# Kernel optimization log

Measured on AMD Instinct MI355X. Metric: run time of the kernel, lower is better.

## Reference

```python
import jax, jax.numpy as jnp
import numpy as np

N_NODES = 3070
N_FEAT = 128
N_OUT = 64
H_SIZE = 50
N_EDGES = 49120
BATCH = 128


def setup_inputs() -> dict:
    key = jax.random.key(0)
    ks = jax.random.split(key, 8)
    x_in = jax.random.normal(ks[0], (BATCH, N_NODES, N_FEAT), dtype=jnp.float32)
    edge_index = jax.random.randint(ks[1], (2, N_EDGES), 0, N_NODES, dtype=jnp.int64)
    edge_weight = jax.random.uniform(ks[2], (N_EDGES,), dtype=jnp.float32)
    W = jax.random.normal(ks[3], (N_FEAT, N_OUT), dtype=jnp.float32) / np.sqrt(N_FEAT)
    b = jnp.zeros((N_OUT,), dtype=jnp.float32)
    W_ih = jax.random.normal(ks[4], (H_SIZE, N_OUT), dtype=jnp.float32) / np.sqrt(N_OUT)
    W_hh = jax.random.normal(ks[5], (H_SIZE, H_SIZE), dtype=jnp.float32) / np.sqrt(H_SIZE)
    b_ih = jnp.zeros((H_SIZE,), dtype=jnp.float32)
    b_hh = jnp.zeros((H_SIZE,), dtype=jnp.float32)
    h0 = jax.random.normal(ks[6], (N_NODES, H_SIZE), dtype=jnp.float32)
    return {"x_in": x_in, "edge_index": edge_index, "edge_weight": edge_weight,
            "W": W, "b": b, "W_ih": W_ih, "W_hh": W_hh, "b_ih": b_ih,
            "b_hh": b_hh, "h0": h0}


def _gcn(x, edge_index, edge_weight, W, b):
    # x: (B, N, F). Vectorized GCNConv over the per-sample python loop.
    n = x.shape[1]
    # vectorized form of the dict-based edge-id remap: rank among unique ids
    uniq = jnp.unique(edge_index, size=n, fill_value=2 ** 30)
    ei = jnp.searchsorted(uniq, edge_index)
    src, dst = ei[0], ei[1]
    # GCNConv default: add self loops with weight 1, symmetric normalization
    loop = jnp.arange(n)
    src = jnp.concatenate([src, loop])
    dst = jnp.concatenate([dst, loop])
    ew = jnp.concatenate([edge_weight, jnp.ones((n,), dtype=x.dtype)])
    deg = jax.ops.segment_sum(ew, dst, num_segments=n)
    dinv = jnp.where(deg > 0, jax.lax.rsqrt(deg), jnp.zeros_like(deg))
    norm = dinv[src] * ew * dinv[dst]                 # (E+N,)
    xw = jnp.einsum('bnf,fo->bno', x, W)              # transform first
    msg = xw[:, src, :] * norm[None, :, None]         # (B, E+N, O)
    out = jnp.zeros_like(xw).at[:, dst, :].add(msg)   # scatter-add to targets
    return out + b


def reference(x_in, edge_index, edge_weight, W, b, W_ih, W_hh, b_ih, b_hh, h0):
    # GCN over all B graph samples (shared fixed graph)
    x = _gcn(x_in, edge_index, edge_weight, W, b)     # (B, N, O)
    # input_horizon==3 -> exactly one horizon step; the torch RNN is seq-first,
    # so seq_len = B (sample dim) and batch = N_NODES, hidden hardcoded 50.
    def step(h, xt):                                   # xt: (N, O), h: (N, H)
        h = jnp.tanh(xt @ W_ih.T + b_ih + h @ W_hh.T + b_hh)
        return h, h
    _, x_out = jax.lax.scan(step, h0, x)               # (B, N, H)
    return x_out
```

## Files before the change

kernel.cpp:

```cpp
#include <hip/hip_runtime.h>

#define NN 3070
#define NF 128
#define NO 64
#define NH 50
#define NC 52
#define NE 49120
#define NB 128
#define MTOT (NB * NN)
#define GCAP 1024
#define NBLK 192
#define GWG2 (NBLK * (NB / 2))
#define GPX2 (GWG2 / 8)

__global__ __launch_bounds__(256) void init_kernel(int* __restrict__ zb,
    const float* __restrict__ W, const float* __restrict__ Wih, const float* __restrict__ b,
    const float* __restrict__ bih, const float* __restrict__ bhh,
    float* __restrict__ Wp, float* __restrict__ bp) {
  int blk = blockIdx.x;
  int tid = threadIdx.x;
  if (blk < 48) {
    int i = blk * 256 + tid;
    if (i < 4 * NN) zb[i] = 0;
    return;
  }
  int idx = (blk - 48) * 256 + tid;
  if (idx < 128 * 64) {
    int k = idx >> 6, j = idx & 63;
    float s = 0.f;
    if (j < NH) {
      for (int o = 0; o < NO; ++o) s += W[k * NO + o] * Wih[j * NO + o];
    }
    Wp[k * 64 + j] = s;
  }
  if (idx < NC) {
    float s = 0.f;
    if (idx < NH) {
      for (int o = 0; o < NO; ++o) s += b[o] * Wih[idx * NO + o];
      s += bih[idx] + bhh[idx];
    }
    bp[idx] = s;
  }
}

__global__ __launch_bounds__(256) void mark_kernel(const int* __restrict__ ei, int* __restrict__ mark) {
  int i = blockIdx.x * 256 + threadIdx.x;
  if (i < 2 * NE) mark[ei[i]] = 1;
}

__global__ __launch_bounds__(1024) void exscan_kernel(const int* __restrict__ in, int* __restrict__ out,
                                                      int n, int write_total, int do_dinv,
                                                      const float* __restrict__ degw,
                                                      float* __restrict__ dinv, float* __restrict__ selfn) {
  __shared__ int part[1024];
  int tid = threadIdx.x;
  int base = tid * 3;
  if (do_dinv) {
#pragma unroll
    for (int u = 0; u < 3; ++u) {
      int nd = base + u;
      if (nd < NN) {
        float dg = degw[nd] + 1.0f;
        float di = rsqrtf(dg);
        dinv[nd] = di;
        selfn[nd] = di * di;
      }
    }
  }
  int v0 = (base + 0 < n) ? in[base + 0] : 0;
  int v1 = (base + 1 < n) ? in[base + 1] : 0;
  int v2 = (base + 2 < n) ? in[base + 2] : 0;
  int s = v0 + v1 + v2;
  part[tid] = s;
  __syncthreads();
  for (int off = 1; off < 1024; off <<= 1) {
    int t = (tid >= off) ? part[tid - off] : 0;
    __syncthreads();
    part[tid] += t;
    __syncthreads();
  }
  int run = part[tid] - s;
  if (base + 0 < n) out[base + 0] = run; run += v0;
  if (base + 1 < n) out[base + 1] = run; run += v1;
  if (base + 2 < n) out[base + 2] = run;
  if (write_total && tid == 1023) out[n] = part[1023];
}

__global__ __launch_bounds__(256) void remap_deg_kernel(const int* __restrict__ ei, const float* __restrict__ ew,
    const int* __restrict__ ranks, int* __restrict__ srcr, int* __restrict__ dstr,
    int* __restrict__ degc, float* __restrict__ degw) {
  int e = blockIdx.x * 256 + threadIdx.x;
  if (e >= NE) return;
  int s = ranks[ei[e]];
  int d = ranks[ei[NE + e]];
  srcr[e] = s;
  dstr[e] = d;
  atomicAdd(&degc[d], 1);
  atomicAdd(&degw[d], ew[e]);
}

__global__ __launch_bounds__(256) void csr_fill_kernel(const float* __restrict__ ew, const int* __restrict__ srcr,
    const int* __restrict__ dstr, const int* __restrict__ rowptr, int* __restrict__ cursor,
    const float* __restrict__ dinv, int* __restrict__ csr_src, float* __restrict__ csr_norm) {
  int e = blockIdx.x * 256 + threadIdx.x;
  if (e >= NE) return;
  int d = dstr[e];
  int s = srcr[e];
  int pos = rowptr[d] + atomicAdd(&cursor[d], 1);
  csr_src[pos] = s;
  csr_norm[pos] = dinv[s] * ew[e] * dinv[d];
}

__global__ __launch_bounds__(256, 3) void gemm_kernel(const float* __restrict__ A,
    const float* __restrict__ W, float* __restrict__ out) {
  __shared__ float As[256 * 36];
  __shared__ float Ws[32 * 64];
  int tid = threadIdx.x;
  int row0 = blockIdx.x * 256;
  int rg = tid >> 3;
  int cg = tid & 7;
  int c0 = cg * 8;
  float acc[8][8];
#pragma unroll
  for (int i = 0; i < 8; ++i)
#pragma unroll
    for (int j = 0; j < 8; ++j) acc[i][j] = 0.f;

  for (int kc = 0; kc < 4; ++kc) {
#pragma unroll
    for (int j = 0; j < 8; ++j) {
      int f = tid + 256 * j;
      int r = f >> 3, kq = f & 7;
      float4 v = *(const float4*)&A[(size_t)(row0 + r) * NF + kc * 32 + kq * 4];
      *(float4*)&As[r * 36 + kq * 4] = v;
    }
#pragma unroll
    for (int j = 0; j < 2; ++j) {
      int f = tid + 256 * j;
      int kk = f >> 4, cq = f & 15;
      *(float4*)&Ws[kk * 64 + cq * 4] = *(const float4*)&W[(size_t)(kc * 32 + kk) * 64 + cq * 4];
    }
    __syncthreads();
#pragma unroll 2
    for (int k4 = 0; k4 < 32; k4 += 4) {
      float4 a[8];
#pragma unroll
      for (int i = 0; i < 8; ++i) a[i] = *(const float4*)&As[(rg + 32 * i) * 36 + k4];
#pragma unroll
      for (int m = 0; m < 4; ++m) {
        float4 w0 = *(const float4*)&Ws[(k4 + m) * 64 + c0];
        float4 w1 = *(const float4*)&Ws[(k4 + m) * 64 + c0 + 4];
#pragma unroll
        for (int i = 0; i < 8; ++i) {
          float av = (m == 0) ? a[i].x : (m == 1) ? a[i].y : (m == 2) ? a[i].z : a[i].w;
          acc[i][0] += av * w0.x; acc[i][1] += av * w0.y;
          acc[i][2] += av * w0.z; acc[i][3] += av * w0.w;
          acc[i][4] += av * w1.x; acc[i][5] += av * w1.y;
          acc[i][6] += av * w1.z; acc[i][7] += av * w1.w;
        }
      }
    }
    __syncthreads();
  }
#pragma unroll
  for (int i = 0; i < 8; ++i) {
    size_t r = row0 + rg + 32 * i;
    if (c0 < NC)
      *(float4*)&out[r * NC + c0] = make_float4(acc[i][0], acc[i][1], acc[i][2], acc[i][3]);
    if (c0 + 4 < NC)
      *(float4*)&out[r * NC + c0 + 4] = make_float4(acc[i][4], acc[i][5], acc[i][6], acc[i][7]);
  }
}

__global__ __launch_bounds__(256) void gather_kernel(const float4* __restrict__ xw,
    const int* __restrict__ rowptr, const int* __restrict__ csr_src, const float* __restrict__ csr_norm,
    const float* __restrict__ selfn, const float* __restrict__ bp, float4* __restrict__ outg) {
  __shared__ int s_src[GCAP];
  __shared__ float s_nrm[GCAP];
  int bid = blockIdx.x;
  int xcd = bid & 7;
  int pos = bid >> 3;
  int work = xcd * GPX2 + pos;
  int bpr = work / NBLK;
  int nblk = work - bpr * NBLK;
  int b0 = bpr * 2;
  int tid = threadIdx.x;
  int f4 = tid & 15, nl = tid >> 4;
  int nb = nblk * 16;
  int nend = nb + 16 < NN ? nb + 16 : NN;
  int be0 = rowptr[nb], be1 = rowptr[nend];
  int cnt = be1 - be0;
  int scnt = cnt < GCAP ? cnt : GCAP;
  for (int i = tid; i < scnt; i += 256) {
    s_src[i] = csr_src[be0 + i];
    s_nrm[i] = csr_norm[be0 + i];
  }
  __syncthreads();
  int n = nb + nl;
  if (n >= NN || f4 >= 13) return;
  const float4* xb0 = xw + (size_t)b0 * NN * 13;
  const float4* xb1 = xb0 + (size_t)NN * 13;
  float sn = selfn[n];
  float4 v0 = xb0[n * 13 + f4];
  float4 v1 = xb1[n * 13 + f4];
  float ax = v0.x * sn, ay = v0.y * sn, az = v0.z * sn, aw = v0.w * sn;
  float bx = 0.f, by = 0.f, bz = 0.f, bw = 0.f;
  float cx = v1.x * sn, cy = v1.y * sn, cz = v1.z * sn, cw = v1.w * sn;
  float dx = 0.f, dy = 0.f, dz = 0.f, dw = 0.f;
  int le0 = rowptr[n] - be0, le1 = rowptr[n + 1] - be0;
  int lim = le1 < GCAP ? le1 : GCAP;
  int e = le0;
  for (; e + 1 < lim; e += 2) {
    int s1 = s_src[e], s2 = s_src[e + 1];
    float w1 = s_nrm[e], w2 = s_nrm[e + 1];
    float4 u10 = xb0[s1 * 13 + f4];
    float4 u20 = xb0[s2 * 13 + f4];
    float4 u11 = xb1[s1 * 13 + f4];
    float4 u21 = xb1[s2 * 13 + f4];
    ax += w1 * u10.x; ay += w1 * u10.y; az += w1 * u10.z; aw += w1 * u10.w;
    bx += w2 * u20.x; by += w2 * u20.y; bz += w2 * u20.z; bw += w2 * u20.w;
    cx += w1 * u11.x; cy += w1 * u11.y; cz += w1 * u11.z; cw += w1 * u11.w;
    dx += w2 * u21.x; dy += w2 * u21.y; dz += w2 * u21.z; dw += w2 * u21.w;
  }
  if (e < lim) {
    int s1 = s_src[e];
    float w1 = s_nrm[e];
    float4 u10 = xb0[s1 * 13 + f4];
    float4 u11 = xb1[s1 * 13 + f4];
    ax += w1 * u10.x; ay += w1 * u10.y; az += w1 * u10.z; aw += w1 * u10.w;
    cx += w1 * u11.x; cy += w1 * u11.y; cz += w1 * u11.z; cw += w1 * u11.w;
  }
  for (e = (le0 > GCAP ? le0 : GCAP); e < le1; ++e) {
    int s1 = csr_src[be0 + e];
    float w1 = csr_norm[be0 + e];
    float4 u10 = xb0[s1 * 13 + f4];
    float4 u11 = xb1[s1 * 13 + f4];
    ax += w1 * u10.x; ay += w1 * u10.y; az += w1 * u10.z; aw += w1 * u10.w;
    cx += w1 * u11.x; cy += w1 * u11.y; cz += w1 * u11.z; cw += w1 * u11.w;
  }
  float4 bb = ((const float4*)bp)[f4];
  float4 o0 = make_float4(ax + bx + bb.x, ay + by + bb.y, az + bz + bb.z, aw + bw + bb.w);
  float4 o1 = make_float4(cx + dx + bb.x, cy + dy + bb.y, cz + dz + bb.z, cw + dw + bb.w);
  outg[((size_t)b0 * NN + n) * 13 + f4] = o0;
  outg[((size_t)(b0 + 1) * NN + n) * 13 + f4] = o1;
}

__global__ __launch_bounds__(256, 3) void rnn_kernel(const float* __restrict__ pre,
    const float* __restrict__ Whh, const float* __restrict__ h0, float* __restrict__ out) {
  __shared__ float hs[6 * 52];
  int tid = threadIdx.x;
  int n0 = blockIdx.x * 5;
  int nl = tid / 50;
  int j = tid - nl * 50;
  bool active = tid < 250;
  int jj = active ? j : 0;
  float2 whh2[25];
  const float2* whhp = (const float2*)(Whh + jj * NH);
#pragma unroll
  for (int q = 0; q < 25; ++q) whh2[q] = whhp[q];
  if (tid < 6 * 52) hs[tid] = 0.f;
  if (tid + 256 < 6 * 52) hs[tid + 256] = 0.f;
  __syncthreads();
  if (active) hs[nl * 52 + j] = h0[n0 * 50 + tid];
  const size_t NPRE = (size_t)NN * NC;
  const size_t NOUT = (size_t)NN * NH;
  int nn = active ? (n0 + nl) : n0;
  const float* prep = pre + (size_t)nn * NC + jj;
  float xpre = prep[0];
  __syncthreads();
  for (int t = 0; t < NB; ++t) {
    float a0 = xpre, a1 = 0.f, a2 = 0.f, a3 = 0.f;
    if (t + 1 < NB) xpre = prep[(size_t)(t + 1) * NPRE];
    const float4* hr = (const float4*)&hs[nl * 52];
#pragma unroll
    for (int q = 0; q < 12; q += 4) {
      float4 h0v = hr[q], h1v = hr[q + 1], h2v = hr[q + 2], h3v = hr[q + 3];
      a0 += h0v.x * whh2[2*q].x   + h0v.y * whh2[2*q].y   + h0v.z * whh2[2*q+1].x + h0v.w * whh2[2*q+1].y;
      a1 += h1v.x * whh2[2*q+2].x + h1v.y * whh2[2*q+2].y + h1v.z * whh2[2*q+3].x + h1v.w * whh2[2*q+3].y;
      a2 += h2v.x * whh2[2*q+4].x + h2v.y * whh2[2*q+4].y + h2v.z * whh2[2*q+5].x + h2v.w * whh2[2*q+5].y;
      a3 += h3v.x * whh2[2*q+6].x + h3v.y * whh2[2*q+6].y + h3v.z * whh2[2*q+7].x + h3v.w * whh2[2*q+7].y;
    }
    {
      float2 ht = *(const float2*)&hs[nl * 52 + 48];
      a0 += ht.x * whh2[24].x + ht.y * whh2[24].y;
    }
    float v = (a0 + a1) + (a2 + a3);
    float e = __expf(-2.f * fabsf(v));
    float r = (1.f - e) * __builtin_amdgcn_rcpf(1.f + e);
    float hnew = (v < 0.f) ? -r : r;
    __syncthreads();
    if (active) {
      hs[nl * 52 + j] = hnew;
      out[(size_t)t * NOUT + n0 * 50 + tid] = hnew;
    }
    __syncthreads();
  }
}


extern "C" void kernel_launch(void* const* d_in, const int* in_sizes, int n_in,
                              void* d_out, int out_size, void* d_ws, size_t ws_size,
                              hipStream_t stream) {
  const float* x_in = (const float*)d_in[0];
  const int* ei     = (const int*)d_in[1];
  const float* ew   = (const float*)d_in[2];
  const float* W    = (const float*)d_in[3];
  const float* bias = (const float*)d_in[4];
  const float* Wih  = (const float*)d_in[5];
  const float* Whh  = (const float*)d_in[6];
  const float* bih  = (const float*)d_in[7];
  const float* bhh  = (const float*)d_in[8];
  const float* h0   = (const float*)d_in[9];
  float* out = (float*)d_out;

  char* ws = (char*)d_ws;
  size_t off = 0;
  auto alloc = [&](size_t bytes) {
    size_t o = off;
    off += (bytes + 255) & ~(size_t)255;
    return o;
  };
  float* xw    = (float*)(ws + alloc((size_t)MTOT * NC * 4));
  float* gcn   = (float*)(ws + alloc((size_t)MTOT * NC * 4));
  int*   zb    = (int*)(ws + alloc((size_t)4 * NN * 4));
  int* mark = zb;
  int* degc = zb + NN;
  float* degw = (float*)(zb + 2 * NN);
  int* cursor = zb + 3 * NN;
  int*   ranks  = (int*)(ws + alloc(NN * 4));
  int*   srcr   = (int*)(ws + alloc(NE * 4));
  int*   dstr   = (int*)(ws + alloc(NE * 4));
  float* dinv   = (float*)(ws + alloc(NN * 4));
  float* selfn  = (float*)(ws + alloc(NN * 4));
  int*   rowptr = (int*)(ws + alloc((NN + 1) * 4));
  int*   csrc   = (int*)(ws + alloc(NE * 4));
  float* cnorm  = (float*)(ws + alloc(NE * 4));
  float* Wp     = (float*)(ws + alloc(128 * 64 * 4));
  float* bp     = (float*)(ws + alloc(NC * 4));

  init_kernel<<<80, 256, 0, stream>>>(zb, W, Wih, bias, bih, bhh, Wp, bp);
  mark_kernel<<<(2 * NE + 255) / 256, 256, 0, stream>>>(ei, mark);
  exscan_kernel<<<1, 1024, 0, stream>>>(mark, ranks, NN, 0, 0, degw, dinv, selfn);
  remap_deg_kernel<<<(NE + 255) / 256, 256, 0, stream>>>(ei, ew, ranks, srcr, dstr, degc, degw);
  exscan_kernel<<<1, 1024, 0, stream>>>(degc, rowptr, NN, 1, 1, degw, dinv, selfn);
  csr_fill_kernel<<<(NE + 255) / 256, 256, 0, stream>>>(ew, srcr, dstr, rowptr, cursor, dinv, csrc, cnorm);

  gemm_kernel<<<MTOT / 256, 256, 0, stream>>>(x_in, Wp, xw);
  gather_kernel<<<GWG2, 256, 0, stream>>>(
      (const float4*)xw, rowptr, csrc, cnorm, selfn, bp, (float4*)gcn);
  rnn_kernel<<<(NN + 4) / 5, 256, 0, stream>>>(gcn, Whh, h0, out);
}
```

Baseline: 536.2 us.

## Stage per-batch feature slice in LDS and gather neighbors from shared memory

```diff
diff --git a/kernel.cpp b/kernel.cpp
--- a/kernel.cpp
+++ b/kernel.cpp
@@ -8,10 +8,8 @@
 #define NE 49120
 #define NB 128
 #define MTOT (NB * NN)
-#define GCAP 1024
-#define NBLK 192
-#define GWG2 (NBLK * (NB / 2))
-#define GPX2 (GWG2 / 8)
+#define GWG3 (7 * NB)
+#define GPX3 (GWG3 / 8)
 
 __global__ __launch_bounds__(256) void init_kernel(int* __restrict__ zb,
     const float* __restrict__ W, const float* __restrict__ Wih, const float* __restrict__ b,
@@ -101,14 +99,14 @@
 
 __global__ __launch_bounds__(256) void csr_fill_kernel(const float* __restrict__ ew, const int* __restrict__ srcr,
     const int* __restrict__ dstr, const int* __restrict__ rowptr, int* __restrict__ cursor,
-    const float* __restrict__ dinv, int* __restrict__ csr_src, float* __restrict__ csr_norm) {
+    const float* __restrict__ dinv, int2* __restrict__ csre) {
   int e = blockIdx.x * 256 + threadIdx.x;
   if (e >= NE) return;
   int d = dstr[e];
   int s = srcr[e];
   int pos = rowptr[d] + atomicAdd(&cursor[d], 1);
-  csr_src[pos] = s;
-  csr_norm[pos] = dinv[s] * ew[e] * dinv[d];
+  float nrm = dinv[s] * ew[e] * dinv[d];
+  csre[pos] = make_int2(2 * s, __float_as_int(nrm));
 }
 
 __global__ __launch_bounds__(256, 3) void gemm_kernel(const float* __restrict__ A,
@@ -172,77 +170,73 @@
   }
 }
 
-__global__ __launch_bounds__(256) void gather_kernel(const float4* __restrict__ xw,
-    const int* __restrict__ rowptr, const int* __restrict__ csr_src, const float* __restrict__ csr_norm,
+__global__ __launch_bounds__(512, 1) void gather_kernel(const float4* __restrict__ xw,
+    const int* __restrict__ rowptr, const int2* __restrict__ csre,
     const float* __restrict__ selfn, const float* __restrict__ bp, float4* __restrict__ outg) {
-  __shared__ int s_src[GCAP];
-  __shared__ float s_nrm[GCAP];
+  __shared__ float4 xls[2 * NN];
   int bid = blockIdx.x;
   int xcd = bid & 7;
   int pos = bid >> 3;
-  int work = xcd * GPX2 + pos;
-  int bpr = work / NBLK;
-  int nblk = work - bpr * NBLK;
-  int b0 = bpr * 2;
-  int tid = threadIdx.x;
-  int f4 = tid & 15, nl = tid >> 4;
-  int nb = nblk * 16;
-  int nend = nb + 16 < NN ? nb + 16 : NN;
-  int be0 = rowptr[nb], be1 = rowptr[nend];
-  int cnt = be1 - be0;
-  int scnt = cnt < GCAP ? cnt : GCAP;
-  for (int i = tid; i < scnt; i += 256) {
-    s_src[i] = csr_src[be0 + i];
-    s_nrm[i] = csr_norm[be0 + i];
+  int work = xcd * GPX3 + pos;
+  int b = work / 7;
+  int p = work - b * 7;
+  int f40 = 2 * p;
+  int tid = threadIdx.x;
+  const float4* xb = xw + (size_t)b * (NN * 13);
+  if (p < 6) {
+    for (int i = tid; i < 2 * NN; i += 512)
+      xls[i] = xb[(i >> 1) * 13 + f40 + (i & 1)];
+  } else {
+    for (int i = tid; i < NN; i += 512)
+      xls[2 * i] = xb[i * 13 + 12];
   }
   __syncthreads();
-  int n = nb + nl;
-  if (n >= NN || f4 >= 13) return;
-  const float4* xb0 = xw + (size_t)b0 * NN * 13;
-  const float4* xb1 = xb0 + (size_t)NN * 13;
-  float sn = selfn[n];
-  float4 v0 = xb0[n * 13 + f4];
-  float4 v1 = xb1[n * 13 + f4];
-  float ax = v0.x * sn, ay = v0.y * sn, az = v0.z * sn, aw = v0.w * sn;
-  float bx = 0.f, by = 0.f, bz = 0.f, bw = 0.f;
-  float cx = v1.x * sn, cy = v1.y * sn, cz = v1.z * sn, cw = v1.w * sn;
-  float dx = 0.f, dy = 0.f, dz = 0.f, dw = 0.f;
-  int le0 = rowptr[n] - be0, le1 = rowptr[n + 1] - be0;
-  int lim = le1 < GCAP ? le1 : GCAP;
-  int e = le0;
-  for (; e + 1 < lim; e += 2) {
-    int s1 = s_src[e], s2 = s_src[e + 1];
-    float w1 = s_nrm[e], w2 = s_nrm[e + 1];
-    float4 u10 = xb0[s1 * 13 + f4];
-    float4 u20 = xb0[s2 * 13 + f4];
-    float4 u11 = xb1[s1 * 13 + f4];
-    float4 u21 = xb1[s2 * 13 + f4];
-    ax += w1 * u10.x; ay += w1 * u10.y; az += w1 * u10.z; aw += w1 * u10.w;
-    bx += w2 * u20.x; by += w2 * u20.y; bz += w2 * u20.z; bw += w2 * u20.w;
-    cx += w1 * u11.x; cy += w1 * u11.y; cz += w1 * u11.z; cw += w1 * u11.w;
-    dx += w2 * u21.x; dy += w2 * u21.y; dz += w2 * u21.z; dw += w2 * u21.w;
-  }
-  if (e < lim) {
-    int s1 = s_src[e];
-    float w1 = s_nrm[e];
-    float4 u10 = xb0[s1 * 13 + f4];
-    float4 u11 = xb1[s1 * 13 + f4];
-    ax += w1 * u10.x; ay += w1 * u10.y; az += w1 * u10.z; aw += w1 * u10.w;
-    cx += w1 * u11.x; cy += w1 * u11.y; cz += w1 * u11.z; cw += w1 * u11.w;
-  }
-  for (e = (le0 > GCAP ? le0 : GCAP); e < le1; ++e) {
-    int s1 = csr_src[be0 + e];
-    float w1 = csr_norm[be0 + e];
-    float4 u10 = xb0[s1 * 13 + f4];
-    float4 u11 = xb1[s1 * 13 + f4];
-    ax += w1 * u10.x; ay += w1 * u10.y; az += w1 * u10.z; aw += w1 * u10.w;
-    cx += w1 * u11.x; cy += w1 * u11.y; cz += w1 * u11.z; cw += w1 * u11.w;
-  }
-  float4 bb = ((const float4*)bp)[f4];
-  float4 o0 = make_float4(ax + bx + bb.x, ay + by + bb.y, az + bz + bb.z, aw + bw + bb.w);
-  float4 o1 = make_float4(cx + dx + bb.x, cy + dy + bb.y, cz + dz + bb.z, cw + dw + bb.w);
-  outg[((size_t)b0 * NN + n) * 13 + f4] = o0;
-  outg[((size_t)(b0 + 1) * NN + n) * 13 + f4] = o1;
+  int n0 = tid * 6;
+  if (n0 >= NN) return;
+  int nend = n0 + 6 <= NN ? n0 + 6 : NN;
+  const float4* bp4 = (const float4*)bp;
+  size_t obase = ((size_t)b * NN) * 13;
+  if (p < 6) {
+    float4 bb0 = bp4[f40], bb1 = bp4[f40 + 1];
+    int e = rowptr[n0];
+    for (int n = n0; n < nend; ++n) {
+      int e1 = rowptr[n + 1];
+      float sn = selfn[n];
+      float4 x0 = xls[2 * n], x1 = xls[2 * n + 1];
+      float a0 = sn * x0.x, a1 = sn * x0.y, a2 = sn * x0.z, a3 = sn * x0.w;
+      float c0 = sn * x1.x, c1 = sn * x1.y, c2 = sn * x1.z, c3 = sn * x1.w;
+#pragma unroll 2
+      for (; e < e1; ++e) {
+        int2 ed = csre[e];
+        float w = __int_as_float(ed.y);
+        float4 u0 = xls[ed.x];
+        float4 u1 = xls[ed.x + 1];
+        a0 += w * u0.x; a1 += w * u0.y; a2 += w * u0.z; a3 += w * u0.w;
+        c0 += w * u1.x; c1 += w * u1.y; c2 += w * u1.z; c3 += w * u1.w;
+      }
+      size_t o = obase + (size_t)n * 13 + f40;
+      outg[o]     = make_float4(a0 + bb0.x, a1 + bb0.y, a2 + bb0.z, a3 + bb0.w);
+      outg[o + 1] = make_float4(c0 + bb1.x, c1 + bb1.y, c2 + bb1.z, c3 + bb1.w);
+    }
+  } else {
+    float4 bb0 = bp4[12];
+    int e = rowptr[n0];
+    for (int n = n0; n < nend; ++n) {
+      int e1 = rowptr[n + 1];
+      float sn = selfn[n];
+      float4 x0 = xls[2 * n];
+      float a0 = sn * x0.x, a1 = sn * x0.y, a2 = sn * x0.z, a3 = sn * x0.w;
+#pragma unroll 2
+      for (; e < e1; ++e) {
+        int2 ed = csre[e];
+        float w = __int_as_float(ed.y);
+        float4 u0 = xls[ed.x];
+        a0 += w * u0.x; a1 += w * u0.y; a2 += w * u0.z; a3 += w * u0.w;
+      }
+      outg[obase + (size_t)n * 13 + 12] =
+          make_float4(a0 + bb0.x, a1 + bb0.y, a2 + bb0.z, a3 + bb0.w);
+    }
+  }
 }
 
 __global__ __launch_bounds__(256, 3) void rnn_kernel(const float* __restrict__ pre,
@@ -333,8 +327,7 @@
   float* dinv   = (float*)(ws + alloc(NN * 4));
   float* selfn  = (float*)(ws + alloc(NN * 4));
   int*   rowptr = (int*)(ws + alloc((NN + 1) * 4));
-  int*   csrc   = (int*)(ws + alloc(NE * 4));
-  float* cnorm  = (float*)(ws + alloc(NE * 4));
+  int2*  csre   = (int2*)(ws + alloc((size_t)NE * 8));
   float* Wp     = (float*)(ws + alloc(128 * 64 * 4));
   float* bp     = (float*)(ws + alloc(NC * 4));
 
@@ -343,10 +336,10 @@
   exscan_kernel<<<1, 1024, 0, stream>>>(mark, ranks, NN, 0, 0, degw, dinv, selfn);
   remap_deg_kernel<<<(NE + 255) / 256, 256, 0, stream>>>(ei, ew, ranks, srcr, dstr, degc, degw);
   exscan_kernel<<<1, 1024, 0, stream>>>(degc, rowptr, NN, 1, 1, degw, dinv, selfn);
-  csr_fill_kernel<<<(NE + 255) / 256, 256, 0, stream>>>(ew, srcr, dstr, rowptr, cursor, dinv, csrc, cnorm);
+  csr_fill_kernel<<<(NE + 255) / 256, 256, 0, stream>>>(ew, srcr, dstr, rowptr, cursor, dinv, csre);
 
   gemm_kernel<<<MTOT / 256, 256, 0, stream>>>(x_in, Wp, xw);
-  gather_kernel<<<GWG2, 256, 0, stream>>>(
-      (const float4*)xw, rowptr, csrc, cnorm, selfn, bp, (float4*)gcn);
+  gather_kernel<<<GWG3, 512, 0, stream>>>(
+      (const float4*)xw, rowptr, csre, selfn, bp, (float4*)gcn);
   rnn_kernel<<<(NN + 4) / 5, 256, 0, stream>>>(gcn, Whh, h0, out);
 }
```

Result: slower. 634.0 us (+18.2%).
